# Kernel tuning notes

Measured on AMD Instinct MI355X. Metric: run time of the kernel, lower is better.

Reference implementation:

```python
import jax, jax.numpy as jnp
import numpy as np

B, S, D = 4, 2048, 1024
H, DK = 16, 64
NUM_BUCKETS = 32
MAX_DISTANCE = 128
EPS = 1e-6


def _relative_position_bucket(q_len, kv_len):
    # causal (bidirectional=False) T5 bucketization
    ctx = jnp.arange(q_len, dtype=jnp.int32)[:, None]
    mem = jnp.arange(kv_len, dtype=jnp.int32)[None, :]
    rp = mem - ctx                       # [q, kv]
    rp = -jnp.minimum(rp, 0)             # nonnegative distances to the past
    max_exact = NUM_BUCKETS // 2
    is_small = rp < max_exact
    rp_safe = jnp.maximum(rp, 1).astype(jnp.float32)
    large = max_exact + (
        jnp.log(rp_safe / max_exact) / np.log(MAX_DISTANCE / max_exact) * (NUM_BUCKETS - max_exact)
    ).astype(jnp.int32)
    large = jnp.minimum(large, NUM_BUCKETS - 1)
    return jnp.where(is_small, rp, large)  # [q, kv] int32 in [0, NUM_BUCKETS)


def setup_inputs() -> dict:
    key = jax.random.key(0)
    k1, k2, k3, k4 = jax.random.split(key, 4)
    hidden_states = jax.random.normal(k1, (B, S, D), dtype=jnp.float32)
    sequence_mask = jnp.ones((B, S), dtype=bool)
    rms_w = jnp.ones((D,), dtype=jnp.float32)
    W_qkv = jax.random.normal(k2, (D, 3 * H * DK), dtype=jnp.float32) * (D ** -0.5)
    W_o = jax.random.normal(k3, (H * DK, D), dtype=jnp.float32) * ((H * DK) ** -0.5)
    rel_bias = jax.random.normal(k4, (NUM_BUCKETS, H), dtype=jnp.float32)
    return {"hidden_states": hidden_states, "sequence_mask": sequence_mask,
            "rms_w": rms_w, "W_qkv": W_qkv, "W_o": W_o, "rel_bias": rel_bias}


def reference(hidden_states, sequence_mask, rms_w, W_qkv, W_o, rel_bias):
    # RMSNorm
    var = jnp.mean(hidden_states * hidden_states, axis=-1, keepdims=True)
    normed = hidden_states * jax.lax.rsqrt(var + EPS) * rms_w

    # QKV projection -> [B, S, 3, H, DK] -> [B, H, S, DK] each
    qkv = (normed @ W_qkv).reshape(B, S, 3, H, DK)
    q = jnp.transpose(qkv[:, :, 0], (0, 2, 1, 3))
    k = jnp.transpose(qkv[:, :, 1], (0, 2, 1, 3))
    v = jnp.transpose(qkv[:, :, 2], (0, 2, 1, 3))

    # relative position bias: gather [S,S,H] -> [1,H,S,S]
    bucket = _relative_position_bucket(S, S)
    pos_bias = jnp.transpose(rel_bias[bucket], (2, 0, 1))[None]

    # scores (note: T5 does NOT scale by 1/sqrt(dk))
    scores = jnp.einsum("bhqd,bhkd->bhqk", q, k) + pos_bias

    # causal mask combined with sequence mask (True = attend)
    causal = jnp.tril(jnp.ones((S, S), dtype=bool))
    mask = causal[None, None] & sequence_mask[:, None, None, :]
    scores = jnp.where(mask, scores, jnp.finfo(scores.dtype).min)

    attn = jax.nn.softmax(scores.astype(jnp.float32), axis=-1).astype(scores.dtype)
    # dropout p=0 / eval mode -> identity
    ctx = jnp.einsum("bhqk,bhkd->bhqd", attn, v)          # [B,H,S,DK]
    ctx = jnp.transpose(ctx, (0, 2, 1, 3)).reshape(B, S, H * DK)
    out = hidden_states + ctx @ W_o                        # residual
    return out
```

## Files before the change

kernel.cpp:

```cpp
#include <hip/hip_runtime.h>
#include <math.h>


typedef unsigned short ushort_t;
typedef __attribute__((ext_vector_type(8))) short bfrag;
typedef __attribute__((ext_vector_type(4))) float ffrag;

#define MFMA16(a, b, c) __builtin_amdgcn_mfma_f32_16x16x32_bf16((a), (b), (c), 0, 0, 0)

__device__ __forceinline__ void load_lds16(const ushort_t* g, ushort_t* l) {
  __builtin_amdgcn_global_load_lds(
      (const __attribute__((address_space(1))) unsigned int*)g,
      (__attribute__((address_space(3))) unsigned int*)l, 16, 0, 0);
}

__device__ __forceinline__ ushort_t f2bf(float f) {
  union { float f; unsigned u; } x; x.f = f;
  unsigned r = x.u + 0x7FFFu + ((x.u >> 16) & 1u);
  return (ushort_t)(r >> 16);
}
__device__ __forceinline__ float bf2f(ushort_t u) {
  union { unsigned u; float f; } x; x.u = ((unsigned)u) << 16; return x.f;
}
__device__ __forceinline__ unsigned pk2bf(float lo, float hi) {
  union { float f; unsigned u; } a, b; a.f = lo; b.f = hi;
  unsigned ra = a.u + 0x7FFFu + ((a.u >> 16) & 1u);
  unsigned rb = b.u + 0x7FFFu + ((b.u >> 16) & 1u);
  return (ra >> 16) | (rb & 0xFFFF0000u);
}

__global__ __launch_bounds__(256) void norm_cvt_kernel(
    const float* __restrict__ hidden, const float* __restrict__ rms_w,
    ushort_t* __restrict__ normed) {
  const int w = threadIdx.x >> 6, lane = threadIdx.x & 63;
  const int row = blockIdx.x * 4 + w;
  const float* p = hidden + (size_t)row * 1024;
  float4 v[4];
  float s = 0.f;
#pragma unroll
  for (int i = 0; i < 4; ++i) {
    v[i] = *(const float4*)(p + (lane + i * 64) * 4);
    s += v[i].x * v[i].x + v[i].y * v[i].y + v[i].z * v[i].z + v[i].w * v[i].w;
  }
#pragma unroll
  for (int off = 1; off < 64; off <<= 1) s += __shfl_xor(s, off, 64);
  const float scale = rsqrtf(s * (1.0f / 1024.0f) + 1e-6f);
#pragma unroll
  for (int i = 0; i < 4; ++i) {
    const int c0 = (lane + i * 64) * 4;
    float4 wv = *(const float4*)(rms_w + c0);
    ushort4 u;
    u.x = f2bf(v[i].x * scale * wv.x);
    u.y = f2bf(v[i].y * scale * wv.y);
    u.z = f2bf(v[i].z * scale * wv.z);
    u.w = f2bf(v[i].w * scale * wv.w);
    *(ushort4*)(normed + (size_t)row * 1024 + c0) = u;
  }
}

__global__ __launch_bounds__(256) void transpose_cvt_kernel(
    const float* __restrict__ in, ushort_t* __restrict__ out, int R, int C) {
  __shared__ float tile[32][33];
  const int r0 = blockIdx.y * 32, c0 = blockIdx.x * 32;
  const int tr = threadIdx.x >> 5, tc = threadIdx.x & 31;
#pragma unroll
  for (int i = 0; i < 32; i += 8)
    tile[tr + i][tc] = in[(size_t)(r0 + tr + i) * C + c0 + tc];
  __syncthreads();
#pragma unroll
  for (int i = 0; i < 32; i += 8)
    out[(size_t)(c0 + tr + i) * R + r0 + tc] = f2bf(tile[tc][tr + i]);
}

__global__ __launch_bounds__(256) void qkv_mfma_kernel(
    const ushort_t* __restrict__ A, const ushort_t* __restrict__ Bt,
    ushort_t* __restrict__ qbf, ushort_t* __restrict__ kbf,
    ushort_t* __restrict__ vtbf) {
  __shared__ ushort_t At[128 * 32];
  __shared__ ushort_t Bs[128 * 32];
  const int tid = threadIdx.x, w = tid >> 6, lane = tid & 63;
  const int quad = lane >> 4, ln = lane & 15;
  const int wr = w >> 1, wc = w & 1;
  const int m0 = blockIdx.y * 128, n0 = blockIdx.x * 128;
  const int srow = lane >> 2, scol = (lane & 3) * 8;

  ffrag acc[4][4];
#pragma unroll
  for (int i = 0; i < 4; ++i)
#pragma unroll
    for (int j = 0; j < 4; ++j) acc[i][j] = (ffrag)0.f;

  for (int kb = 0; kb < 1024; kb += 32) {
#pragma unroll
    for (int p = 0; p < 2; ++p) {
      load_lds16(A + (size_t)(m0 + (w * 2 + p) * 16 + srow) * 1024 + kb + scol,
                 At + (w * 2 + p) * 512);
      load_lds16(Bt + (size_t)(n0 + (w * 2 + p) * 16 + srow) * 1024 + kb + scol,
                 Bs + (w * 2 + p) * 512);
    }
    __syncthreads();
    bfrag a[4], b[4];
#pragma unroll
    for (int mi = 0; mi < 4; ++mi)
      a[mi] = *(const bfrag*)(At + (wr * 64 + mi * 16 + ln) * 32 + quad * 8);
#pragma unroll
    for (int ni = 0; ni < 4; ++ni)
      b[ni] = *(const bfrag*)(Bs + (wc * 64 + ni * 16 + ln) * 32 + quad * 8);
#pragma unroll
    for (int mi = 0; mi < 4; ++mi)
#pragma unroll
      for (int ni = 0; ni < 4; ++ni)
        acc[mi][ni] = MFMA16(a[mi], b[ni], acc[mi][ni]);
    __syncthreads();
  }

  const int b_idx = m0 >> 11;
  const int cbase = n0 + wc * 64 + ln;
#pragma unroll
  for (int mi = 0; mi < 4; ++mi) {
    const int sbase = (m0 & 2047) + wr * 64 + mi * 16 + quad * 4;
#pragma unroll
    for (int ni = 0; ni < 4; ++ni) {
      const int c = cbase + ni * 16;
      const int three = c >> 10, rem = c & 1023;
      const int h = rem >> 6, dk = rem & 63;
      if (three == 2) {
        ushort4 u;
        u.x = f2bf(acc[mi][ni][0]); u.y = f2bf(acc[mi][ni][1]);
        u.z = f2bf(acc[mi][ni][2]); u.w = f2bf(acc[mi][ni][3]);
        *(ushort4*)(vtbf + ((size_t)(b_idx * 16 + h) * 64 + dk) * 2048 + sbase) = u;
      } else {
        ushort_t* dst = (three == 0 ? qbf : kbf) +
                        ((size_t)(b_idx * 16 + h) * 2048 + sbase) * 64 + dk;
        dst[0]   = f2bf(acc[mi][ni][0]);
        dst[64]  = f2bf(acc[mi][ni][1]);
        dst[128] = f2bf(acc[mi][ni][2]);
        dst[192] = f2bf(acc[mi][ni][3]);
      }
    }
  }
}

__global__ __launch_bounds__(256) void attn_mfma_kernel(
    const ushort_t* __restrict__ qbf, const ushort_t* __restrict__ kbf,
    const ushort_t* __restrict__ vtbf, const float* __restrict__ rel_bias,
    ushort_t* __restrict__ ctx) {
  __shared__ ushort_t Kt[2][64][32];
  __shared__ ushort_t Vt[2][64][32];
  __shared__ ushort_t Pt[128][72];
  __shared__ ushort_t bias_t[2048];

  const int tid = threadIdx.x, w = tid >> 6, lane = tid & 63;
  const int quad = lane >> 4, ln = lane & 15;
  const int id = blockIdx.x;
  const int bh = id & 63;
  const int g = id >> 6;
  const int qb = (g < 4) ? (15 - 2 * g)
               : (g < 8) ? (2 * g - 8)
               : (g < 12) ? (30 - 2 * g)
                          : (2 * g - 23);
  const int h = bh & 15;

  for (int dist = tid; dist < 2048; dist += 256) {
    int bucket;
    if (dist < 16) bucket = dist;
    else {
      bucket = 16 + (int)(logf((float)dist * (1.0f / 16.0f)) * (16.0f / logf(8.0f)));
      if (bucket > 31) bucket = 31;
    }
    bias_t[dist] = f2bf(rel_bias[bucket * 16 + h]);
  }
  const float c31 = bf2f(f2bf(rel_bias[31 * 16 + h]));

  const int q0w = qb * 128 + w * 32;
  const size_t qrow = (size_t)bh * 2048 + q0w + ln;
  bfrag aq[2][2];
#pragma unroll
  for (int ni = 0; ni < 2; ++ni)
#pragma unroll
    for (int kf = 0; kf < 2; ++kf)
      aq[ni][kf] = *(const bfrag*)(qbf + (qrow + ni * 16) * 64 + kf * 32 + quad * 8);

  ffrag o[2][4];
  float m_run[2] = {-3.0e38f, -3.0e38f}, l_run[2] = {0.f, 0.f};
#pragma unroll
  for (int mo = 0; mo < 2; ++mo)
#pragma unroll
    for (int nd = 0; nd < 4; ++nd) o[mo][nd] = (ffrag)0.f;

  const int sidx = lane >> 2, scol8 = (lane & 3) * 8;
  const size_t khead = (size_t)bh * 2048 * 64;
  const int jmax = qb * 2 + 1;

  for (int j = 0; j <= jmax; ++j) {
    const int key0 = j * 64;
#pragma unroll
    for (int p = 0; p < 2; ++p) {
      const int idx = p * 4 + w, panel = idx >> 2, rb = idx & 3;
      load_lds16(kbf + khead + (size_t)(key0 + rb * 16 + sidx) * 64 + panel * 32 + scol8,
                 &Kt[0][0][0] + idx * 512);
      load_lds16(vtbf + khead + (size_t)(rb * 16 + sidx) * 2048 + key0 + panel * 32 + scol8,
                 &Vt[0][0][0] + idx * 512);
    }
    __syncthreads();

    if (key0 <= q0w + 31) {
      ffrag s[4][2];
#pragma unroll
      for (int mi = 0; mi < 4; ++mi)
#pragma unroll
        for (int ni = 0; ni < 2; ++ni) s[mi][ni] = (ffrag)0.f;
#pragma unroll
      for (int kf = 0; kf < 2; ++kf)
#pragma unroll
        for (int mi = 0; mi < 4; ++mi) {
          bfrag ak = *(const bfrag*)&Kt[kf][mi * 16 + ln][quad * 8];
          s[mi][0] = MFMA16(ak, aq[0][kf], s[mi][0]);
          s[mi][1] = MFMA16(ak, aq[1][kf], s[mi][1]);
        }

      float alpha[2];
      const bool fast = (key0 + 176 <= q0w);
      if (fast) {
#pragma unroll
        for (int ni = 0; ni < 2; ++ni) {
          float mx = s[0][ni][0];
#pragma unroll
          for (int mi = 0; mi < 4; ++mi)
#pragma unroll
            for (int r = 0; r < 4; ++r) mx = fmaxf(mx, s[mi][ni][r]);
          mx = fmaxf(mx, __shfl_xor(mx, 16, 64));
          mx = fmaxf(mx, __shfl_xor(mx, 32, 64));
          const float mnew = fmaxf(m_run[ni], mx + c31);
          alpha[ni] = __expf(m_run[ni] - mnew);
          const float sh = mnew - c31;
          float ps = 0.f;
#pragma unroll
          for (int mi = 0; mi < 4; ++mi)
#pragma unroll
            for (int r = 0; r < 4; ++r) {
              const float pv = __expf(s[mi][ni][r] - sh);
              s[mi][ni][r] = pv;
              ps += pv;
            }
          ps += __shfl_xor(ps, 16, 64);
          ps += __shfl_xor(ps, 32, 64);
          l_run[ni] = l_run[ni] * alpha[ni] + ps;
          m_run[ni] = mnew;
        }
      } else {
#pragma unroll
        for (int ni = 0; ni < 2; ++ni) {
          const int q = q0w + ni * 16 + ln;
          float mx = -3.0e38f;
#pragma unroll
          for (int mi = 0; mi < 4; ++mi) {
            const int keyb = key0 + mi * 16 + quad * 4;
#pragma unroll
            for (int r = 0; r < 4; ++r) {
              const int dist = q - (keyb + r);
              const float val =
                  (dist < 0) ? -3.0e38f : (s[mi][ni][r] + bf2f(bias_t[dist]));
              s[mi][ni][r] = val;
              mx = fmaxf(mx, val);
            }
          }
          mx = fmaxf(mx, __shfl_xor(mx, 16, 64));
          mx = fmaxf(mx, __shfl_xor(mx, 32, 64));
          const float mnew = fmaxf(m_run[ni], mx);
          alpha[ni] = __expf(m_run[ni] - mnew);
          float ps = 0.f;
#pragma unroll
          for (int mi = 0; mi < 4; ++mi)
#pragma unroll
            for (int r = 0; r < 4; ++r) {
              const float pv = __expf(s[mi][ni][r] - mnew);
              s[mi][ni][r] = pv;
              ps += pv;
            }
          ps += __shfl_xor(ps, 16, 64);
          ps += __shfl_xor(ps, 32, 64);
          l_run[ni] = l_run[ni] * alpha[ni] + ps;
          m_run[ni] = mnew;
        }
      }

#pragma unroll
      for (int ni = 0; ni < 2; ++ni) {
        ushort_t* prow = &Pt[w * 32 + ni * 16 + ln][0];
#pragma unroll
        for (int mi = 0; mi < 4; ++mi) {
          uint2 pk;
          pk.x = pk2bf(s[mi][ni][0], s[mi][ni][1]);
          pk.y = pk2bf(s[mi][ni][2], s[mi][ni][3]);
          *(uint2*)(prow + mi * 16 + quad * 4) = pk;
        }
      }

#pragma unroll
      for (int mo = 0; mo < 2; ++mo) {
#pragma unroll
        for (int r = 0; r < 4; ++r) {
          const float af = __shfl(alpha[mo], quad * 4 + r, 64);
#pragma unroll
          for (int nd = 0; nd < 4; ++nd) o[mo][nd][r] *= af;
        }
      }

#pragma unroll
      for (int kf = 0; kf < 2; ++kf) {
        bfrag ap0 = *(const bfrag*)&Pt[w * 32 + ln][kf * 32 + quad * 8];
        bfrag ap1 = *(const bfrag*)&Pt[w * 32 + 16 + ln][kf * 32 + quad * 8];
#pragma unroll
        for (int nd = 0; nd < 4; ++nd) {
          bfrag bv = *(const bfrag*)&Vt[kf][nd * 16 + ln][quad * 8];
          o[0][nd] = MFMA16(ap0, bv, o[0][nd]);
          o[1][nd] = MFMA16(ap1, bv, o[1][nd]);
        }
      }
    }
    __syncthreads();
  }

#pragma unroll
  for (int mo = 0; mo < 2; ++mo) {
    ffrag inv;
#pragma unroll
    for (int r = 0; r < 4; ++r)
      inv[r] = 1.0f / __shfl(l_run[mo], quad * 4 + r, 64);
    const int s0 = q0w + mo * 16 + quad * 4;
#pragma unroll
    for (int nd = 0; nd < 4; ++nd)
#pragma unroll
      for (int r = 0; r < 4; ++r)
        ctx[((size_t)(bh >> 4) * 2048 + s0 + r) * 1024 + h * 64 + nd * 16 + ln] =
            f2bf(o[mo][nd][r] * inv[r]);
  }
}

__global__ __launch_bounds__(256) void out_mfma_kernel(
    const ushort_t* __restrict__ A, const ushort_t* __restrict__ Bt,
    const float* __restrict__ hidden, float* __restrict__ out) {
  __shared__ ushort_t At[128 * 32];
  __shared__ ushort_t Bs[128 * 32];
  const int tid = threadIdx.x, w = tid >> 6, lane = tid & 63;
  const int quad = lane >> 4, ln = lane & 15;
  const int wr = w >> 1, wc = w & 1;
  const int m0 = blockIdx.y * 128, n0 = blockIdx.x * 128;
  const int srow = lane >> 2, scol = (lane & 3) * 8;

  ffrag acc[4][4];
#pragma unroll
  for (int i = 0; i < 4; ++i)
#pragma unroll
    for (int j = 0; j < 4; ++j) acc[i][j] = (ffrag)0.f;

  for (int kb = 0; kb < 1024; kb += 32) {
#pragma unroll
    for (int p = 0; p < 2; ++p) {
      load_lds16(A + (size_t)(m0 + (w * 2 + p) * 16 + srow) * 1024 + kb + scol,
                 At + (w * 2 + p) * 512);
      load_lds16(Bt + (size_t)(n0 + (w * 2 + p) * 16 + srow) * 1024 + kb + scol,
                 Bs + (w * 2 + p) * 512);
    }
    __syncthreads();
    bfrag a[4], b[4];
#pragma unroll
    for (int mi = 0; mi < 4; ++mi)
      a[mi] = *(const bfrag*)(At + (wr * 64 + mi * 16 + ln) * 32 + quad * 8);
#pragma unroll
    for (int ni = 0; ni < 4; ++ni)
      b[ni] = *(const bfrag*)(Bs + (wc * 64 + ni * 16 + ln) * 32 + quad * 8);
#pragma unroll
    for (int mi = 0; mi < 4; ++mi)
#pragma unroll
      for (int ni = 0; ni < 4; ++ni)
        acc[mi][ni] = MFMA16(a[mi], b[ni], acc[mi][ni]);
    __syncthreads();
  }
#pragma unroll
  for (int mi = 0; mi < 4; ++mi) {
    const int m = m0 + wr * 64 + mi * 16 + quad * 4;
#pragma unroll
    for (int ni = 0; ni < 4; ++ni) {
      const int c = n0 + wc * 64 + ni * 16 + ln;
#pragma unroll
      for (int r = 0; r < 4; ++r) {
        const size_t off = (size_t)(m + r) * 1024 + c;
        out[off] = acc[mi][ni][r] + hidden[off];
      }
    }
  }
}

extern "C" void kernel_launch(void* const* d_in, const int* in_sizes, int n_in,
                              void* d_out, int out_size, void* d_ws, size_t ws_size,
                              hipStream_t stream) {
  const size_t NORMED = (size_t)8192 * 1024;
  const size_t WQKVT  = (size_t)3072 * 1024;
  const size_t WOT    = (size_t)1024 * 1024;
  const size_t QKVE   = (size_t)64 * 2048 * 64;
  const size_t need = (NORMED + WQKVT + WOT + 3 * QKVE + NORMED) * 2;
  if (ws_size < need) return;

  const float* hidden   = (const float*)d_in[0];
  const float* rms_w    = (const float*)d_in[2];
  const float* Wqkv     = (const float*)d_in[3];
  const float* Wo       = (const float*)d_in[4];
  const float* rel_bias = (const float*)d_in[5];
  float* out = (float*)d_out;

  ushort_t* normed = (ushort_t*)d_ws;
  ushort_t* wqkvt  = normed + NORMED;
  ushort_t* wot    = wqkvt + WQKVT;
  ushort_t* qbf    = wot + WOT;
  ushort_t* kbf    = qbf + QKVE;
  ushort_t* vtbf   = kbf + QKVE;
  ushort_t* ctx    = vtbf + QKVE;

  norm_cvt_kernel<<<2048, 256, 0, stream>>>(hidden, rms_w, normed);
  transpose_cvt_kernel<<<dim3(96, 32), 256, 0, stream>>>(Wqkv, wqkvt, 1024, 3072);
  transpose_cvt_kernel<<<dim3(32, 32), 256, 0, stream>>>(Wo, wot, 1024, 1024);
  qkv_mfma_kernel<<<dim3(24, 64), 256, 0, stream>>>(normed, wqkvt, qbf, kbf, vtbf);
  attn_mfma_kernel<<<1024, 256, 0, stream>>>(qbf, kbf, vtbf, rel_bias, ctx);
  out_mfma_kernel<<<dim3(8, 64), 256, 0, stream>>>(ctx, wot, hidden, out);
}
```

Before: 309.6 us.

## Restructure causal attention into paired 64-row query tiles with exp2 and swizzled LDS

Each attention block now processes two 64-row query tiles (qb and 31-qb) in sequence instead of one 128-row tile, so every block gets the same amount of causal work, and each wave handles 16 query rows. K is pre-scaled by log2(e) in the QKV epilogue and the bias table is stored as fp32 pre-scaled, so softmax can use a hardware exp2 intrinsic. LDS reads and writes for K, V and P use XOR swizzles to cut bank conflicts, and the P buffer shrinks. The cost is that each K/V tile is now shared by fewer query rows, so K/V loads per unit of compute go up, and the bias is no longer rounded through bf16.

```diff
diff --git a/kernel.cpp b/kernel.cpp
--- a/kernel.cpp
+++ b/kernel.cpp
@@ -7,6 +7,7 @@
 typedef __attribute__((ext_vector_type(4))) float ffrag;
 
 #define MFMA16(a, b, c) __builtin_amdgcn_mfma_f32_16x16x32_bf16((a), (b), (c), 0, 0, 0)
+#define LOG2E 1.4426950408889634f
 
 __device__ __forceinline__ void load_lds16(const ushort_t* g, ushort_t* l) {
   __builtin_amdgcn_global_load_lds(
@@ -18,15 +19,15 @@
   union { float f; unsigned u; } x; x.f = f;
   unsigned r = x.u + 0x7FFFu + ((x.u >> 16) & 1u);
   return (ushort_t)(r >> 16);
-}
-__device__ __forceinline__ float bf2f(ushort_t u) {
-  union { unsigned u; float f; } x; x.u = ((unsigned)u) << 16; return x.f;
 }
 __device__ __forceinline__ unsigned pk2bf(float lo, float hi) {
   union { float f; unsigned u; } a, b; a.f = lo; b.f = hi;
   unsigned ra = a.u + 0x7FFFu + ((a.u >> 16) & 1u);
   unsigned rb = b.u + 0x7FFFu + ((b.u >> 16) & 1u);
   return (ra >> 16) | (rb & 0xFFFF0000u);
+}
+__device__ __forceinline__ float exp2fast(float x) {
+  return __builtin_amdgcn_exp2f(x);
 }
 
 __global__ __launch_bounds__(256) void norm_cvt_kernel(
@@ -130,12 +131,13 @@
         u.z = f2bf(acc[mi][ni][2]); u.w = f2bf(acc[mi][ni][3]);
         *(ushort4*)(vtbf + ((size_t)(b_idx * 16 + h) * 64 + dk) * 2048 + sbase) = u;
       } else {
+        const float sc = (three == 0) ? 1.0f : LOG2E;
         ushort_t* dst = (three == 0 ? qbf : kbf) +
                         ((size_t)(b_idx * 16 + h) * 2048 + sbase) * 64 + dk;
-        dst[0]   = f2bf(acc[mi][ni][0]);
-        dst[64]  = f2bf(acc[mi][ni][1]);
-        dst[128] = f2bf(acc[mi][ni][2]);
-        dst[192] = f2bf(acc[mi][ni][3]);
+        dst[0]   = f2bf(acc[mi][ni][0] * sc);
+        dst[64]  = f2bf(acc[mi][ni][1] * sc);
+        dst[128] = f2bf(acc[mi][ni][2] * sc);
+        dst[192] = f2bf(acc[mi][ni][3] * sc);
       }
     }
   }
@@ -147,18 +149,14 @@
     ushort_t* __restrict__ ctx) {
   __shared__ ushort_t Kt[2][64][32];
   __shared__ ushort_t Vt[2][64][32];
-  __shared__ ushort_t Pt[128][72];
-  __shared__ ushort_t bias_t[2048];
+  __shared__ ushort_t Pt[64][64];
+  __shared__ float bias_f[2048];
 
   const int tid = threadIdx.x, w = tid >> 6, lane = tid & 63;
   const int quad = lane >> 4, ln = lane & 15;
   const int id = blockIdx.x;
   const int bh = id & 63;
-  const int g = id >> 6;
-  const int qb = (g < 4) ? (15 - 2 * g)
-               : (g < 8) ? (2 * g - 8)
-               : (g < 12) ? (30 - 2 * g)
-                          : (2 * g - 23);
+  const int pr = id >> 6;
   const int h = bh & 15;
 
   for (int dist = tid; dist < 2048; dist += 256) {
@@ -168,173 +166,153 @@
       bucket = 16 + (int)(logf((float)dist * (1.0f / 16.0f)) * (16.0f / logf(8.0f)));
       if (bucket > 31) bucket = 31;
     }
-    bias_t[dist] = f2bf(rel_bias[bucket * 16 + h]);
-  }
-  const float c31 = bf2f(f2bf(rel_bias[31 * 16 + h]));
-
-  const int q0w = qb * 128 + w * 32;
-  const size_t qrow = (size_t)bh * 2048 + q0w + ln;
-  bfrag aq[2][2];
-#pragma unroll
-  for (int ni = 0; ni < 2; ++ni)
+    bias_f[dist] = rel_bias[bucket * 16 + h] * LOG2E;
+  }
+  const float c31 = rel_bias[31 * 16 + h] * LOG2E;
+
+  const size_t khead = (size_t)bh * 2048 * 64;
+  const int sidx = lane >> 2;
+  const int scol8 = ((lane & 3) ^ ((lane >> 3) & 3)) * 8;
+  const int rsw = ((ln >> 1) & 3) * 8;
+  const int psw = (ln & 7) * 8;
+
+  for (int ph = 0; ph < 2; ++ph) {
+    const int qb = ph ? (31 - pr) : pr;
+    const int q0w = qb * 64 + w * 16;
+
+    bfrag aq[2];
 #pragma unroll
     for (int kf = 0; kf < 2; ++kf)
-      aq[ni][kf] = *(const bfrag*)(qbf + (qrow + ni * 16) * 64 + kf * 32 + quad * 8);
-
-  ffrag o[2][4];
-  float m_run[2] = {-3.0e38f, -3.0e38f}, l_run[2] = {0.f, 0.f};
-#pragma unroll
-  for (int mo = 0; mo < 2; ++mo)
-#pragma unroll
-    for (int nd = 0; nd < 4; ++nd) o[mo][nd] = (ffrag)0.f;
-
-  const int sidx = lane >> 2, scol8 = (lane & 3) * 8;
-  const size_t khead = (size_t)bh * 2048 * 64;
-  const int jmax = qb * 2 + 1;
-
-  for (int j = 0; j <= jmax; ++j) {
-    const int key0 = j * 64;
-#pragma unroll
-    for (int p = 0; p < 2; ++p) {
-      const int idx = p * 4 + w, panel = idx >> 2, rb = idx & 3;
-      load_lds16(kbf + khead + (size_t)(key0 + rb * 16 + sidx) * 64 + panel * 32 + scol8,
-                 &Kt[0][0][0] + idx * 512);
-      load_lds16(vtbf + khead + (size_t)(rb * 16 + sidx) * 2048 + key0 + panel * 32 + scol8,
-                 &Vt[0][0][0] + idx * 512);
-    }
-    __syncthreads();
-
-    if (key0 <= q0w + 31) {
-      ffrag s[4][2];
-#pragma unroll
-      for (int mi = 0; mi < 4; ++mi)
-#pragma unroll
-        for (int ni = 0; ni < 2; ++ni) s[mi][ni] = (ffrag)0.f;
+      aq[kf] = *(const bfrag*)(qbf + ((size_t)bh * 2048 + q0w + ln) * 64 +
+                               kf * 32 + quad * 8);
+
+    ffrag o[4];
+#pragma unroll
+    for (int nd = 0; nd < 4; ++nd) o[nd] = (ffrag)0.f;
+    float m_run = -3.0e38f, l_run = 0.f;
+
+    for (int j = 0; j <= qb; ++j) {
+      const int key0 = j * 64;
+#pragma unroll
+      for (int p2 = 0; p2 < 2; ++p2) {
+        load_lds16(kbf + khead + (size_t)(key0 + w * 16 + sidx) * 64 + p2 * 32 + scol8,
+                   &Kt[0][0][0] + (p2 * 4 + w) * 512);
+        load_lds16(vtbf + khead + (size_t)(w * 16 + sidx) * 2048 + key0 + p2 * 32 + scol8,
+                   &Vt[0][0][0] + (p2 * 4 + w) * 512);
+      }
+      __syncthreads();
+
+      ffrag s[4];
+#pragma unroll
+      for (int mi = 0; mi < 4; ++mi) s[mi] = (ffrag)0.f;
 #pragma unroll
       for (int kf = 0; kf < 2; ++kf)
 #pragma unroll
         for (int mi = 0; mi < 4; ++mi) {
-          bfrag ak = *(const bfrag*)&Kt[kf][mi * 16 + ln][quad * 8];
-          s[mi][0] = MFMA16(ak, aq[0][kf], s[mi][0]);
-          s[mi][1] = MFMA16(ak, aq[1][kf], s[mi][1]);
+          bfrag ak = *(const bfrag*)&Kt[kf][mi * 16 + ln][(quad * 8) ^ rsw];
+          s[mi] = MFMA16(ak, aq[kf], s[mi]);
         }
 
-      float alpha[2];
-      const bool fast = (key0 + 176 <= q0w);
-      if (fast) {
-#pragma unroll
-        for (int ni = 0; ni < 2; ++ni) {
-          float mx = s[0][ni][0];
-#pragma unroll
-          for (int mi = 0; mi < 4; ++mi)
-#pragma unroll
-            for (int r = 0; r < 4; ++r) mx = fmaxf(mx, s[mi][ni][r]);
-          mx = fmaxf(mx, __shfl_xor(mx, 16, 64));
-          mx = fmaxf(mx, __shfl_xor(mx, 32, 64));
-          const float mnew = fmaxf(m_run[ni], mx + c31);
-          alpha[ni] = __expf(m_run[ni] - mnew);
-          const float sh = mnew - c31;
-          float ps = 0.f;
-#pragma unroll
-          for (int mi = 0; mi < 4; ++mi)
-#pragma unroll
-            for (int r = 0; r < 4; ++r) {
-              const float pv = __expf(s[mi][ni][r] - sh);
-              s[mi][ni][r] = pv;
-              ps += pv;
-            }
-          ps += __shfl_xor(ps, 16, 64);
-          ps += __shfl_xor(ps, 32, 64);
-          l_run[ni] = l_run[ni] * alpha[ni] + ps;
-          m_run[ni] = mnew;
+      float alpha;
+      if (key0 + 176 <= q0w) {
+        float mx = s[0][0];
+#pragma unroll
+        for (int mi = 0; mi < 4; ++mi)
+#pragma unroll
+          for (int r = 0; r < 4; ++r) mx = fmaxf(mx, s[mi][r]);
+        mx = fmaxf(mx, __shfl_xor(mx, 16, 64));
+        mx = fmaxf(mx, __shfl_xor(mx, 32, 64));
+        const float mnew = fmaxf(m_run, mx + c31);
+        alpha = exp2fast(m_run - mnew);
+        const float sh = mnew - c31;
+        float ps = 0.f;
+#pragma unroll
+        for (int mi = 0; mi < 4; ++mi)
+#pragma unroll
+          for (int r = 0; r < 4; ++r) {
+            const float pv = exp2fast(s[mi][r] - sh);
+            s[mi][r] = pv;
+            ps += pv;
+          }
+        ps += __shfl_xor(ps, 16, 64);
+        ps += __shfl_xor(ps, 32, 64);
+        l_run = l_run * alpha + ps;
+        m_run = mnew;
+      } else {
+        const int q = q0w + ln;
+        float mx = -3.0e38f;
+#pragma unroll
+        for (int mi = 0; mi < 4; ++mi) {
+          const int keyb = key0 + mi * 16 + quad * 4;
+#pragma unroll
+          for (int r = 0; r < 4; ++r) {
+            const int dist = q - (keyb + r);
+            const int db = dist < 0 ? 0 : dist;
+            const float val = (dist < 0) ? -3.0e38f : (s[mi][r] + bias_f[db]);
+            s[mi][r] = val;
+            mx = fmaxf(mx, val);
+          }
         }
-      } else {
-#pragma unroll
-        for (int ni = 0; ni < 2; ++ni) {
-          const int q = q0w + ni * 16 + ln;
-          float mx = -3.0e38f;
-#pragma unroll
-          for (int mi = 0; mi < 4; ++mi) {
-            const int keyb = key0 + mi * 16 + quad * 4;
-#pragma unroll
-            for (int r = 0; r < 4; ++r) {
-              const int dist = q - (keyb + r);
-              const float val =
-                  (dist < 0) ? -3.0e38f : (s[mi][ni][r] + bf2f(bias_t[dist]));
-              s[mi][ni][r] = val;
-              mx = fmaxf(mx, val);
-            }
+        mx = fmaxf(mx, __shfl_xor(mx, 16, 64));
+        mx = fmaxf(mx, __shfl_xor(mx, 32, 64));
+        const float mnew = fmaxf(m_run, mx);
+        alpha = exp2fast(m_run - mnew);
+        float ps = 0.f;
+#pragma unroll
+        for (int mi = 0; mi < 4; ++mi)
+#pragma unroll
+          for (int r = 0; r < 4; ++r) {
+            const float pv = exp2fast(s[mi][r] - mnew);
+            s[mi][r] = pv;
+            ps += pv;
           }
-          mx = fmaxf(mx, __shfl_xor(mx, 16, 64));
-          mx = fmaxf(mx, __shfl_xor(mx, 32, 64));
-          const float mnew = fmaxf(m_run[ni], mx);
-          alpha[ni] = __expf(m_run[ni] - mnew);
-          float ps = 0.f;
-#pragma unroll
-          for (int mi = 0; mi < 4; ++mi)
-#pragma unroll
-            for (int r = 0; r < 4; ++r) {
-              const float pv = __expf(s[mi][ni][r] - mnew);
-              s[mi][ni][r] = pv;
-              ps += pv;
-            }
-          ps += __shfl_xor(ps, 16, 64);
-          ps += __shfl_xor(ps, 32, 64);
-          l_run[ni] = l_run[ni] * alpha[ni] + ps;
-          m_run[ni] = mnew;
-        }
-      }
-
-#pragma unroll
-      for (int ni = 0; ni < 2; ++ni) {
-        ushort_t* prow = &Pt[w * 32 + ni * 16 + ln][0];
+        ps += __shfl_xor(ps, 16, 64);
+        ps += __shfl_xor(ps, 32, 64);
+        l_run = l_run * alpha + ps;
+        m_run = mnew;
+      }
+
+      {
+        ushort_t* prow = &Pt[w * 16 + ln][0];
 #pragma unroll
         for (int mi = 0; mi < 4; ++mi) {
           uint2 pk;
-          pk.x = pk2bf(s[mi][ni][0], s[mi][ni][1]);
-          pk.y = pk2bf(s[mi][ni][2], s[mi][ni][3]);
-          *(uint2*)(prow + mi * 16 + quad * 4) = pk;
+          pk.x = pk2bf(s[mi][0], s[mi][1]);
+          pk.y = pk2bf(s[mi][2], s[mi][3]);
+          *(uint2*)(prow + ((mi * 16 + quad * 4) ^ psw)) = pk;
         }
       }
 
 #pragma unroll
-      for (int mo = 0; mo < 2; ++mo) {
-#pragma unroll
-        for (int r = 0; r < 4; ++r) {
-          const float af = __shfl(alpha[mo], quad * 4 + r, 64);
-#pragma unroll
-          for (int nd = 0; nd < 4; ++nd) o[mo][nd][r] *= af;
+      for (int r = 0; r < 4; ++r) {
+        const float af = __shfl(alpha, quad * 4 + r, 64);
+#pragma unroll
+        for (int nd = 0; nd < 4; ++nd) o[nd][r] *= af;
+      }
+
+#pragma unroll
+      for (int kf = 0; kf < 2; ++kf) {
+        bfrag ap = *(const bfrag*)&Pt[w * 16 + ln][(kf * 32 + quad * 8) ^ psw];
+#pragma unroll
+        for (int nd = 0; nd < 4; ++nd) {
+          bfrag bv = *(const bfrag*)&Vt[kf][nd * 16 + ln][(quad * 8) ^ rsw];
+          o[nd] = MFMA16(ap, bv, o[nd]);
         }
       }
-
-#pragma unroll
-      for (int kf = 0; kf < 2; ++kf) {
-        bfrag ap0 = *(const bfrag*)&Pt[w * 32 + ln][kf * 32 + quad * 8];
-        bfrag ap1 = *(const bfrag*)&Pt[w * 32 + 16 + ln][kf * 32 + quad * 8];
-#pragma unroll
-        for (int nd = 0; nd < 4; ++nd) {
-          bfrag bv = *(const bfrag*)&Vt[kf][nd * 16 + ln][quad * 8];
-          o[0][nd] = MFMA16(ap0, bv, o[0][nd]);
-          o[1][nd] = MFMA16(ap1, bv, o[1][nd]);
-        }
-      }
-    }
-    __syncthreads();
-  }
-
-#pragma unroll
-  for (int mo = 0; mo < 2; ++mo) {
+      __syncthreads();
+    }
+
     ffrag inv;
 #pragma unroll
     for (int r = 0; r < 4; ++r)
-      inv[r] = 1.0f / __shfl(l_run[mo], quad * 4 + r, 64);
-    const int s0 = q0w + mo * 16 + quad * 4;
+      inv[r] = 1.0f / __shfl(l_run, quad * 4 + r, 64);
+    const int s0 = q0w + quad * 4;
 #pragma unroll
     for (int nd = 0; nd < 4; ++nd)
 #pragma unroll
       for (int r = 0; r < 4; ++r)
         ctx[((size_t)(bh >> 4) * 2048 + s0 + r) * 1024 + h * 64 + nd * 16 + ln] =
-            f2bf(o[mo][nd][r] * inv[r]);
+            f2bf(o[nd][r] * inv[r]);
   }
 }
 
```

Result: no change. 314.0 us (+1.4%).
